# Kernel optimization log

Measured on AMD Instinct MI355X. Metric: run time of the kernel, lower is better.

## Reference

```python
import jax, jax.numpy as jnp
import numpy as np

DIM = 1536
RMS_EPS = 1e-7
LN_EPS = 1e-5


def rmsnorm(x, w):
    ms = jnp.mean(x * x, axis=-1, keepdims=True)
    return x / jnp.sqrt(ms + RMS_EPS) * w


def layernorm(x, w, b):
    mu = jnp.mean(x, axis=-1, keepdims=True)
    var = jnp.mean((x - mu) ** 2, axis=-1, keepdims=True)
    return (x - mu) / jnp.sqrt(var + LN_EPS) * w + b


def linear(x, W, b):
    # W stored as (in, out)
    return jnp.einsum('bnd,df->bnf', x, W) + b


def setup_inputs() -> dict:
    key = jax.random.key(0)
    ks = jax.random.split(key, 32)
    D = DIM
    s = 0.02
    inp = {
        'x': jax.random.normal(ks[0], (2, 4096, D), jnp.float32),
        'text_emb': jax.random.normal(ks[1], (2, 512, D), jnp.float32),
        # norm params
        'sq_w': jnp.ones((D,), jnp.float32),
        'sk_w': jnp.ones((D,), jnp.float32),
        'cq_w': jnp.ones((D,), jnp.float32),
        'ck_w': jnp.ones((D,), jnp.float32),
        'ln_w': jnp.ones((D,), jnp.float32),
        'ln_b': jnp.zeros((D,), jnp.float32),
        # self-attn projections
        'Wq': jax.random.normal(ks[2], (D, D), jnp.float32) * s,
        'bq': jnp.zeros((D,), jnp.float32),
        'Wk': jax.random.normal(ks[3], (D, D), jnp.float32) * s,
        'bk': jnp.zeros((D,), jnp.float32),
        'Wv': jax.random.normal(ks[4], (D, D), jnp.float32) * s,
        'bv': jnp.zeros((D,), jnp.float32),
        'Wo': jax.random.normal(ks[5], (D, D), jnp.float32) * s,
        'bo': jnp.zeros((D,), jnp.float32),
        # cross-attn projections
        'CWq': jax.random.normal(ks[6], (D, D), jnp.float32) * s,
        'Cbq': jnp.zeros((D,), jnp.float32),
        'CWk': jax.random.normal(ks[7], (D, D), jnp.float32) * s,
        'Cbk': jnp.zeros((D,), jnp.float32),
        'CWv': jax.random.normal(ks[8], (D, D), jnp.float32) * s,
        'Cbv': jnp.zeros((D,), jnp.float32),
        'CWo': jax.random.normal(ks[9], (D, D), jnp.float32) * s,
        'Cbo': jnp.zeros((D,), jnp.float32),
        # FFN
        'W1': jax.random.normal(ks[10], (D, 4 * D), jnp.float32) * s,
        'b1': jnp.zeros((4 * D,), jnp.float32),
        'W2': jax.random.normal(ks[11], (4 * D, D), jnp.float32) * s,
        'b2': jnp.zeros((D,), jnp.float32),
    }
    return inp


def reference(x, text_emb, sq_w, sk_w, cq_w, ck_w, ln_w, ln_b,
              Wq, bq, Wk, bk, Wv, bv, Wo, bo,
              CWq, Cbq, CWk, Cbk, CWv, Cbv, CWo, Cbo,
              W1, b1, W2, b2):
    scale = 1.0 / jnp.sqrt(jnp.float32(DIM))  # NOTE: full-dim scale, no head split (faithful)

    # self-attention (single-head over full dim)
    q = linear(rmsnorm(x, sq_w), Wq, bq)
    k = linear(rmsnorm(x, sk_w), Wk, bk)
    v = linear(x, Wv, bv)
    attn = jax.nn.softmax(jnp.einsum('bnd,bmd->bnm', q, k) * scale, axis=-1)
    attn_out = linear(jnp.einsum('bnm,bmd->bnd', attn, v), Wo, bo)

    # cross-attention
    cq = linear(rmsnorm(x, cq_w), CWq, Cbq)
    ck = linear(rmsnorm(text_emb, ck_w), CWk, Cbk)
    cv = linear(text_emb, CWv, Cbv)
    cattn = jax.nn.softmax(jnp.einsum('bnd,bmd->bnm', cq, ck) * scale, axis=-1)
    cross_out = linear(jnp.einsum('bnm,bmd->bnd', cattn, cv), CWo, Cbo)

    # FFN with exact GELU (torch nn.GELU default)
    h = linear(layernorm(x, ln_w, ln_b), W1, b1)
    ffn_out = linear(jax.nn.gelu(h, approximate=False), W2, b2)

    return x + attn_out + cross_out + ffn_out
```

## Files before the change

### kernel.cpp

```cpp
#include <hip/hip_runtime.h>
#include <hip/hip_bf16.h>
#include <cmath>

#define DD 1536
#define FF 6144

typedef __bf16 bf16_t;
typedef __bf16 bf16x8 __attribute__((ext_vector_type(8)));
typedef __bf16 bf16x4 __attribute__((ext_vector_type(4)));
typedef float  f32x4  __attribute__((ext_vector_type(4)));

#define VM0 asm volatile("s_waitcnt vmcnt(0)" ::: "memory")
#define SB  __builtin_amdgcn_sched_barrier(0)
#define LGKM_0 do { asm volatile("s_waitcnt lgkmcnt(0)" :::); SB; } while (0)
#define LGKM_4 do { asm volatile("s_waitcnt lgkmcnt(4)" :::); SB; } while (0)
#define BAR __builtin_amdgcn_s_barrier()

__device__ __forceinline__ void async_load16(const bf16_t* g, bf16_t* l) {
  __builtin_amdgcn_global_load_lds(
      (const __attribute__((address_space(1))) void*)g,
      (__attribute__((address_space(3))) void*)l, 16, 0, 0);
}

__device__ __forceinline__ bf16x8 ds_read128(unsigned int addr) {
  bf16x8 r;
  asm volatile("ds_read_b128 %0, %1" : "=v"(r) : "v"(addr));
  return r;
}

__device__ __forceinline__ void xcd_remap(int& bx, int& by) {
  const int gx = gridDim.x, gy = gridDim.y;
  int wg = by * gx + bx;
  const int nwg = gx * gy;
  const int q = nwg >> 3, r = nwg & 7, xcd = wg & 7, o = wg >> 3;
  wg = (xcd < r ? xcd * (q + 1) : r * (q + 1) + (xcd - r) * q) + o;
  bx = wg % gx;
  by = wg / gx;
}

__global__ __launch_bounds__(256) void transpose_to_bf16(
    const float* __restrict__ W, bf16_t* __restrict__ Wt, int K, int N,
    const float* __restrict__ s, int ldt) {
  __shared__ float tile[32][33];
  const int tx = threadIdx.x, ty = threadIdx.y;
  const int n0 = blockIdx.x * 32, k0 = blockIdx.y * 32;
#pragma unroll
  for (int i = 0; i < 4; i++)
    tile[ty + 8 * i][tx] = W[(size_t)(k0 + ty + 8 * i) * N + n0 + tx];
  __syncthreads();
  const float sc = (s != nullptr) ? s[k0 + tx] : 1.f;
#pragma unroll
  for (int i = 0; i < 4; i++)
    Wt[(size_t)(n0 + ty + 8 * i) * ldt + k0 + tx] = (bf16_t)(tile[tx][ty + 8 * i] * sc);
}

__global__ __launch_bounds__(256) void bias_add2(
    const float* __restrict__ a, const float* __restrict__ b, float* __restrict__ o, int n) {
  const int i = blockIdx.x * 256 + threadIdx.x;
  if (i < n) o[i] = a[i] + b[i];
}

__device__ __forceinline__ void breduce1(float& a) {
#pragma unroll
  for (int off = 32; off; off >>= 1) a += __shfl_xor(a, off);
  __shared__ float sa[4];
  const int w = threadIdx.x >> 6, ln = threadIdx.x & 63;
  if (ln == 0) sa[w] = a;
  __syncthreads();
  a = (sa[0] + sa[1]) + (sa[2] + sa[3]);
  __syncthreads();
}

__device__ __forceinline__ void breduce2(float& a, float& b) {
#pragma unroll
  for (int off = 32; off; off >>= 1) {
    a += __shfl_xor(a, off);
    b += __shfl_xor(b, off);
  }
  __shared__ float sa[4], sb[4];
  const int w = threadIdx.x >> 6, ln = threadIdx.x & 63;
  if (ln == 0) { sa[w] = a; sb[w] = b; }
  __syncthreads();
  a = (sa[0] + sa[1]) + (sa[2] + sa[3]);
  b = (sb[0] + sb[1]) + (sb[2] + sb[3]);
  __syncthreads();
}

__global__ __launch_bounds__(256) void norm_x1(
    const float* __restrict__ x, bf16_t* __restrict__ xr, float* __restrict__ rqinv) {
  const int row = blockIdx.x, t = threadIdx.x;
  const float* p = x + (size_t)row * DD;
  f32x4 v0 = ((const f32x4*)p)[t];
  f32x4 v1 = 0.0f;
  if (t < 128) v1 = ((const f32x4*)p)[256 + t];
  float s2 = 0.f;
#pragma unroll
  for (int e = 0; e < 4; e++) s2 += v0[e] * v0[e];
  if (t < 128) {
#pragma unroll
    for (int e = 0; e < 4; e++) s2 += v1[e] * v1[e];
  }
  breduce1(s2);
  const float ms = s2 * (1.f / DD) + 1e-7f;
  const float rq = rsqrtf(ms);
  if (t == 0) rqinv[row] = sqrtf(ms);
  auto emit = [&](int ci, f32x4 v) {
    bf16x4 orr;
#pragma unroll
    for (int e = 0; e < 4; e++) orr[e] = (bf16_t)(v[e] * rq);
    *(bf16x4*)(xr + (size_t)row * DD + ci * 4) = orr;
  };
  emit(t, v0);
  if (t < 128) emit(256 + t, v1);
}

__global__ __launch_bounds__(256) void norm_ln(
    const float* __restrict__ x, const float* __restrict__ w,
    const float* __restrict__ bb, bf16_t* __restrict__ o) {
  const int row = blockIdx.x, t = threadIdx.x;
  const float* p = x + (size_t)row * DD;
  f32x4 v0 = ((const f32x4*)p)[t];
  f32x4 v1 = 0.0f;
  if (t < 128) v1 = ((const f32x4*)p)[256 + t];
  float s = 0.f, s2 = 0.f;
#pragma unroll
  for (int e = 0; e < 4; e++) { s += v0[e]; s2 += v0[e] * v0[e]; }
  if (t < 128) {
#pragma unroll
    for (int e = 0; e < 4; e++) { s += v1[e]; s2 += v1[e] * v1[e]; }
  }
  breduce2(s, s2);
  const float mu = s * (1.f / DD);
  const float rln = rsqrtf(s2 * (1.f / DD) - mu * mu + 1e-5f);
  auto emit = [&](int ci, f32x4 v) {
    const int i0 = ci * 4;
    bf16x4 ov;
#pragma unroll
    for (int e = 0; e < 4; e++)
      ov[e] = (bf16_t)((v[e] - mu) * rln * w[i0 + e] + bb[i0 + e]);
    *(bf16x4*)(o + (size_t)row * DD + i0) = ov;
  };
  emit(t, v0);
  if (t < 128) emit(256 + t, v1);
}

__global__ __launch_bounds__(256) void norm_t2(
    const float* __restrict__ te, bf16_t* __restrict__ tb, bf16_t* __restrict__ tck) {
  const int row = blockIdx.x, t = threadIdx.x;
  const float* p = te + (size_t)row * DD;
  f32x4 v0 = ((const f32x4*)p)[t];
  f32x4 v1 = 0.0f;
  if (t < 128) v1 = ((const f32x4*)p)[256 + t];
  float s2 = 0.f;
#pragma unroll
  for (int e = 0; e < 4; e++) s2 += v0[e] * v0[e];
  if (t < 128) {
#pragma unroll
    for (int e = 0; e < 4; e++) s2 += v1[e] * v1[e];
  }
  breduce1(s2);
  const float rq = rsqrtf(s2 * (1.f / DD) + 1e-7f);
  auto emit = [&](int ci, f32x4 v) {
    bf16x4 ob, oc;
#pragma unroll
    for (int e = 0; e < 4; e++) {
      ob[e] = (bf16_t)v[e];
      oc[e] = (bf16_t)(v[e] * rq);
    }
    const size_t o = (size_t)row * DD + ci * 4;
    *(bf16x4*)(tb + o) = ob;
    *(bf16x4*)(tck + o) = oc;
  };
  emit(t, v0);
  if (t < 128) emit(256 + t, v1);
}

template <int NC>
__global__ __launch_bounds__(256) void softmax_bf16(bf16_t* __restrict__ S) {
  const int t = threadIdx.x;
  bf16_t* sr = S + (size_t)blockIdx.x * NC;
  constexpr int NV = (NC / 8 + 255) / 256;
  float v[NV][8];
  float mx = -3.4e38f;
#pragma unroll
  for (int i = 0; i < NV; i++) {
    const int idx = t + i * 256;
    if (idx * 8 < NC) {
      bf16x8 b = ((const bf16x8*)sr)[idx];
#pragma unroll
      for (int e = 0; e < 8; e++) {
        v[i][e] = (float)b[e];
        mx = fmaxf(mx, v[i][e]);
      }
    }
  }
#pragma unroll
  for (int off = 32; off; off >>= 1) mx = fmaxf(mx, __shfl_xor(mx, off));
  __shared__ float sm[4];
  const int w = t >> 6, ln = t & 63;
  if (ln == 0) sm[w] = mx;
  __syncthreads();
  mx = fmaxf(fmaxf(sm[0], sm[1]), fmaxf(sm[2], sm[3]));
  __syncthreads();
  float sum = 0.f;
#pragma unroll
  for (int i = 0; i < NV; i++) {
    const int idx = t + i * 256;
    if (idx * 8 < NC) {
#pragma unroll
      for (int e = 0; e < 8; e++) {
        v[i][e] = __expf(v[i][e] - mx);
        sum += v[i][e];
      }
    }
  }
#pragma unroll
  for (int off = 32; off; off >>= 1) sum += __shfl_xor(sum, off);
  __shared__ float ss[4];
  if (ln == 0) ss[w] = sum;
  __syncthreads();
  sum = (ss[0] + ss[1]) + (ss[2] + ss[3]);
  const float inv = 1.f / sum;
#pragma unroll
  for (int i = 0; i < NV; i++) {
    const int idx = t + i * 256;
    if (idx * 8 < NC) {
      bf16x8 o;
#pragma unroll
      for (int e = 0; e < 8; e++) o[e] = (bf16_t)(v[i][e] * inv);
      ((bf16x8*)sr)[idx] = o;
    }
  }
}

enum { EPI_BF16 = 0, EPI_F32_SCALE = 1, EPI_ADD_X = 2, EPI_ACC = 3, EPI_GELU = 4, EPI_TRANS = 5, EPI_BF16S = 6, EPI_PROJ3 = 7 };

template <int EPI>
__device__ __forceinline__ void epi_frag(
    f32x4 v, int r0, int c, const float* bias, void* Cout, const float* Xres,
    int ldc, float scale, int t_ld, int t_bshift, size_t t_bstride) {
  const float bv = (bias != nullptr) ? bias[c] : 0.f;
  if constexpr (EPI == EPI_BF16) {
    bf16_t* C = (bf16_t*)Cout;
#pragma unroll
    for (int r = 0; r < 4; r++) C[(size_t)(r0 + r) * ldc + c] = (bf16_t)(v[r] + bv);
  } else if constexpr (EPI == EPI_F32_SCALE) {
    float* C = (float*)Cout;
#pragma unroll
    for (int r = 0; r < 4; r++) C[(size_t)(r0 + r) * ldc + c] = v[r] * scale;
  } else if constexpr (EPI == EPI_BF16S) {
    bf16_t* C = (bf16_t*)Cout;
#pragma unroll
    for (int r = 0; r < 4; r++) C[(size_t)(r0 + r) * ldc + c] = (bf16_t)(v[r] * scale);
  } else if constexpr (EPI == EPI_ADD_X) {
    float* C = (float*)Cout;
#pragma unroll
    for (int r = 0; r < 4; r++) {
      const size_t ix = (size_t)(r0 + r) * ldc + c;
      C[ix] = Xres[ix] + v[r] + bv;
    }
  } else if constexpr (EPI == EPI_ACC) {
    float* C = (float*)Cout;
#pragma unroll
    for (int r = 0; r < 4; r++) {
      const size_t ix = (size_t)(r0 + r) * ldc + c;
      C[ix] += v[r] + bv;
    }
  } else if constexpr (EPI == EPI_GELU) {
    bf16_t* C = (bf16_t*)Cout;
#pragma unroll
    for (int r = 0; r < 4; r++) {
      const float h = v[r] + bv;
      C[(size_t)(r0 + r) * ldc + c] = (bf16_t)(0.5f * h * (1.f + erff(h * 0.70710678118654752f)));
    }
  } else if constexpr (EPI == EPI_TRANS) {
    const int b = r0 >> t_bshift;
    const int n = r0 & ((1 << t_bshift) - 1);
    bf16_t* C = (bf16_t*)Cout + (size_t)b * t_bstride + (size_t)c * t_ld + n;
    bf16x4 o;
#pragma unroll
    for (int r = 0; r < 4; r++) o[r] = (bf16_t)(v[r] + bv);
    *(bf16x4*)C = o;
  } else {
    bf16_t* base = (bf16_t*)Cout;
    if (c < 1536) {
      const int b = r0 >> 12, n = r0 & 4095;
      bf16_t* C = base + 25165824 + (size_t)b * ((size_t)DD * 4096) + (size_t)c * 4096 + n;
      bf16x4 o;
#pragma unroll
      for (int r = 0; r < 4; r++) o[r] = (bf16_t)(v[r] * Xres[r0 + r] + bv);
      *(bf16x4*)C = o;
    } else if (c < 4608) {
#pragma unroll
      for (int r = 0; r < 4; r++) base[(size_t)(r0 + r) * 3072 + (c - 1536)] = (bf16_t)(v[r] + bv);
    } else {
      bf16_t* C = base + 37748736;
#pragma unroll
      for (int r = 0; r < 4; r++) C[(size_t)(r0 + r) * 1536 + (c - 4608)] = (bf16_t)(v[r] + bv);
    }
  }
}

template <int EPI>
__global__ __launch_bounds__(256) void gemm_bt(
    const bf16_t* __restrict__ A, const bf16_t* __restrict__ B,
    const float* __restrict__ bias, void* __restrict__ Cout,
    const float* __restrict__ Xres,
    int nK, int lda, int ldb, int ldc, float scale,
    int bsh, size_t bstr, int t_ld, int t_bshift, size_t t_bstride) {
  __shared__ __align__(16) bf16_t As[2][128 * 32];
  __shared__ __align__(16) bf16_t Bs[2][128 * 32];
  const int tid = threadIdx.x;
  int bx = blockIdx.x, by = blockIdx.y;
  xcd_remap(bx, by);
  const int m0 = by * 128, n0 = bx * 128;
  const int wave = tid >> 6, lane = tid & 63, l15 = lane & 15, hi = lane >> 4;
  const int wm = wave >> 1, wn = wave & 1;
  const int srow = tid >> 2, scol = (tid & 3) << 3;

  const bf16_t* Bb = bsh ? (B + (size_t)(m0 >> bsh) * bstr) : B;
  const bf16_t* ga = A + (size_t)(m0 + srow) * lda + scol;
  const bf16_t* gb = Bb + (size_t)(n0 + srow) * ldb + scol;
  const int lo = wave * 512;

  f32x4 acc[4][4];
#pragma unroll
  for (int i = 0; i < 4; i++)
#pragma unroll
    for (int j = 0; j < 4; j++) acc[i][j] = 0.0f;

  auto stage = [&](int buf, int kt) {
    const bf16_t* a = ga + (size_t)kt * 32;
    const bf16_t* b = gb + (size_t)kt * 32;
    async_load16(a, &As[buf][lo]);
    async_load16(a + (size_t)64 * lda, &As[buf][2048 + lo]);
    async_load16(b, &Bs[buf][lo]);
    async_load16(b + (size_t)64 * ldb, &Bs[buf][2048 + lo]);
  };

  auto compute = [&](int buf) {
    bf16x8 af[4], bg[4];
#pragma unroll
    for (int i = 0; i < 4; i++)
      af[i] = *(const bf16x8*)&As[buf][(wm * 64 + i * 16 + l15) * 32 + hi * 8];
#pragma unroll
    for (int j = 0; j < 4; j++)
      bg[j] = *(const bf16x8*)&Bs[buf][(wn * 64 + j * 16 + l15) * 32 + hi * 8];
#pragma unroll
    for (int i = 0; i < 4; i++)
#pragma unroll
      for (int j = 0; j < 4; j++)
        acc[i][j] = __builtin_amdgcn_mfma_f32_16x16x32_bf16(af[i], bg[j], acc[i][j], 0, 0, 0);
  };

  stage(0, 0);
  __syncthreads();
  for (int kt = 0; kt < nK; ++kt) {
    if (kt + 1 < nK) stage((kt + 1) & 1, kt + 1);
    compute(kt & 1);
    __syncthreads();
  }

#pragma unroll
  for (int i = 0; i < 4; i++) {
    const int r0 = m0 + wm * 64 + i * 16 + hi * 4;
#pragma unroll
    for (int j = 0; j < 4; j++) {
      const int c = n0 + wn * 64 + j * 16 + l15;
      epi_frag<EPI>(acc[i][j], r0, c, bias, Cout, Xres, ldc, scale, t_ld, t_bshift, t_bstride);
    }
  }
}

template <int EPI>
__global__ __launch_bounds__(512, 2) void gemm8(
    const bf16_t* __restrict__ A, const bf16_t* __restrict__ B,
    const float* __restrict__ bias, void* __restrict__ Cout,
    const float* __restrict__ Xres,
    int nT, int lda, int ldb, int ldc, float scale,
    int bsh, size_t bstr, int t_ld, int t_bshift, size_t t_bstride) {
  __shared__ __align__(16) bf16_t As[2][256 * 64];
  __shared__ __align__(16) bf16_t Bs[2][256 * 64];
  const int tid = threadIdx.x;
  int bx = blockIdx.x, by = blockIdx.y;
  xcd_remap(bx, by);
  const int m0 = by * 256, n0 = bx * 256;
  const int wave = tid >> 6, lane = tid & 63, l15 = lane & 15, hi = lane >> 4;
  const int wm = wave >> 2, wn = wave & 3;

  const int srow = tid >> 3;
  const int scol = ((tid & 7) ^ (srow & 7)) << 3;
  const bf16_t* Bb = bsh ? (B + (size_t)(m0 >> bsh) * bstr) : B;
  const bf16_t* gA = A + (size_t)(m0 + srow) * lda + scol;
  const bf16_t* gB = Bb + (size_t)(n0 + srow) * ldb + scol;
  const int ldst = wave * 512;

  const unsigned swz0 = (unsigned)(((hi ^ (l15 & 7)) << 3) * 2);
  const unsigned swz1 = (unsigned)((((hi + 4) ^ (l15 & 7)) << 3) * 2);
  const unsigned aBase = (unsigned)(size_t)&As[0][0] + (unsigned)((wm * 128 + l15) * 128);
  const unsigned bBase = (unsigned)(size_t)&Bs[0][0] + (unsigned)((wn * 64 + l15) * 128);
  const unsigned a0 = aBase + swz0, a1 = aBase + swz1;
  const unsigned b0 = bBase + swz0, b1 = bBase + swz1;

  f32x4 acc[8][4];
#pragma unroll
  for (int i = 0; i < 8; i++)
#pragma unroll
    for (int j = 0; j < 4; j++) acc[i][j] = 0.0f;

  auto stgA = [&](int t, int half) {
    if (t >= nT) return;
    const int buf = t & 1, r0 = half << 7;
    const size_t kof = (size_t)t * 64;
    async_load16(gA + (size_t)r0 * lda + kof, &As[buf][r0 * 64 + ldst]);
    async_load16(gA + (size_t)(r0 + 64) * lda + kof, &As[buf][(r0 + 64) * 64 + ldst]);
  };
  auto stgB = [&](int t, int half) {
    if (t >= nT) return;
    const int buf = t & 1, r0 = half << 7;
    const size_t kof = (size_t)t * 64;
    async_load16(gB + (size_t)r0 * ldb + kof, &Bs[buf][r0 * 64 + ldst]);
    async_load16(gB + (size_t)(r0 + 64) * ldb + kof, &Bs[buf][(r0 + 64) * 64 + ldst]);
  };

  bf16x8 af[4][2], bg[2][2][2];
  auto LDA = [&](int buf, int mh) {
#pragma unroll
    for (int i = 0; i < 4; i++) {
      const unsigned d = (unsigned)(buf * 32768 + (mh * 4 + i) * 2048);
      af[i][0] = ds_read128(a0 + d);
      af[i][1] = ds_read128(a1 + d);
    }
  };
  auto LDB = [&](int buf, int nh) {
#pragma unroll
    for (int j = 0; j < 2; j++) {
      const unsigned d = (unsigned)(buf * 32768 + (nh * 2 + j) * 2048);
      bg[nh][j][0] = ds_read128(b0 + d);
      bg[nh][j][1] = ds_read128(b1 + d);
    }
  };
  auto MM = [&](int mh, int nh) {
    __builtin_amdgcn_s_setprio(1);
#pragma unroll
    for (int i = 0; i < 4; i++)
#pragma unroll
      for (int j = 0; j < 2; j++)
#pragma unroll
        for (int ks = 0; ks < 2; ks++)
          acc[mh * 4 + i][nh * 2 + j] = __builtin_amdgcn_mfma_f32_16x16x32_bf16(
              af[i][ks], bg[nh][j][ks], acc[mh * 4 + i][nh * 2 + j], 0, 0, 0);
    __builtin_amdgcn_s_setprio(0);
  };

  auto iter = [&](int k, int buf) {
    VM0;
    BAR;
    stgB(k + 1, 0);
    stgB(k + 1, 1);
    stgA(k + 1, 0);
    stgA(k + 1, 1);
    LDA(buf, 0);
    LDB(buf, 0);
    LDB(buf, 1);
    SB;
    LGKM_4;
    MM(0, 0);
    LGKM_0;
    MM(0, 1);
    LDA(buf, 1);
    SB;
    LGKM_0;
    MM(1, 0);
    MM(1, 1);
  };

  stgB(0, 0); stgB(0, 1); stgA(0, 0); stgA(0, 1);

  for (int k = 0; k < nT; k += 2) {
    iter(k, 0);
    iter(k + 1, 1);
  }

#pragma unroll
  for (int fi = 0; fi < 8; fi++) {
    const int r0 = m0 + wm * 128 + fi * 16 + hi * 4;
#pragma unroll
    for (int fj = 0; fj < 4; fj++) {
      const int c = n0 + wn * 64 + fj * 16 + l15;
      epi_frag<EPI>(acc[fi][fj], r0, c, bias, Cout, Xres, ldc, scale, t_ld, t_bshift, t_bstride);
    }
  }
}

extern "C" void kernel_launch(void* const* d_in, const int* in_sizes, int n_in,
                              void* d_out, int out_size, void* d_ws, size_t ws_size,
                              hipStream_t stream) {
  (void)in_sizes; (void)n_in; (void)out_size; (void)ws_size;
  const float* x   = (const float*)d_in[0];
  const float* te  = (const float*)d_in[1];
  const float* sqw = (const float*)d_in[2];
  const float* skw = (const float*)d_in[3];
  const float* cqw = (const float*)d_in[4];
  const float* ckw = (const float*)d_in[5];
  const float* lnw = (const float*)d_in[6];
  const float* lnb = (const float*)d_in[7];
  const float* Wq = (const float*)d_in[8];  const float* bq = (const float*)d_in[9];
  const float* Wk = (const float*)d_in[10]; const float* bk = (const float*)d_in[11];
  const float* Wv = (const float*)d_in[12]; const float* bv = (const float*)d_in[13];
  const float* Wo = (const float*)d_in[14]; const float* bo = (const float*)d_in[15];
  const float* CWq = (const float*)d_in[16]; const float* Cbq = (const float*)d_in[17];
  const float* CWk = (const float*)d_in[18]; const float* Cbk = (const float*)d_in[19];
  const float* CWv = (const float*)d_in[20]; const float* Cbv = (const float*)d_in[21];
  const float* CWo = (const float*)d_in[22]; const float* Cbo = (const float*)d_in[23];
  const float* W1 = (const float*)d_in[24]; const float* b1 = (const float*)d_in[25];
  const float* W2 = (const float*)d_in[26]; const float* b2 = (const float*)d_in[27];
  float* out = (float*)d_out;

  bf16_t* ws = (bf16_t*)d_ws;
  bf16_t* R0 = ws;
  bf16_t* R1 = ws + 9437184;
  bf16_t* R2 = ws + 18874368;
  bf16_t* Tb  = ws + 31457280;
  bf16_t* Tck = ws + 33030144;
  bf16_t* R4 = ws + 34603008;
  bf16_t* R5 = ws + 59768832;
  bf16_t* R6 = ws + 72351744;
  bf16_t* S  = ws;
  float* bcat4 = (float*)(ws + 84934656);
  float* biasm = (float*)(ws + 84946944);
  float* rqinv = (float*)(ws + 84950016);
  bf16_t* CK  = R0;
  bf16_t* CVt = R0 + 1572864;
  bf16_t* Sc  = R0 + 3145728;
  bf16_t* H   = R4;

  const dim3 blk(256), blk8(512), tb(32, 8);
  const float scl = 0.025515518153991442f;

  auto T = [&](const float* W, bf16_t* Wt, int K, int N, const float* s, int ldt) {
    transpose_to_bf16<<<dim3(N / 32, K / 32), tb, 0, stream>>>(W, Wt, K, N, s, ldt);
  };
  auto g8 = [](int M, int N) { return dim3(N / 256, M / 256); };
  auto g4 = [](int M, int N) { return dim3(N / 128, M / 128); };

  hipMemcpyAsync(bcat4,        bv,  DD * sizeof(float), hipMemcpyDeviceToDevice, stream);
  hipMemcpyAsync(bcat4 + DD,   bq,  DD * sizeof(float), hipMemcpyDeviceToDevice, stream);
  hipMemcpyAsync(bcat4 + 2*DD, bk,  DD * sizeof(float), hipMemcpyDeviceToDevice, stream);
  hipMemcpyAsync(bcat4 + 3*DD, Cbq, DD * sizeof(float), hipMemcpyDeviceToDevice, stream);
  bias_add2<<<6, blk, 0, stream>>>(bo, Cbo, biasm, DD);

  norm_x1<<<8192, blk, 0, stream>>>(x, R2, rqinv);

  T(Wv,  R0,               DD, DD, nullptr, DD);
  T(Wq,  R0 + 2359296,     DD, DD, sqw,     DD);
  T(Wk,  R0 + 4718592,     DD, DD, skw,     DD);
  T(CWq, R0 + 7077888,     DD, DD, cqw,     DD);
  gemm8<EPI_PROJ3><<<g8(8192, FF), blk8, 0, stream>>>(R2, R0, bcat4, R4, rqinv,
      24, DD, DD, 3072, 1.f, 0, 0, 0, 0, 0);

  gemm8<EPI_BF16S><<<g8(8192, 4096), blk8, 0, stream>>>(R4 , R4 + DD , nullptr, S, nullptr,
      24, 3072, 3072, 4096, scl, 12, (size_t)4096 * 3072, 0, 0, 0);
  softmax_bf16<4096><<<8192, blk, 0, stream>>>(S);
  gemm8<EPI_BF16><<<g8(8192, DD), blk8, 0, stream>>>(S, R5, nullptr, R4, nullptr,
      64, 4096, 4096, 3072, 1.f, 12, (size_t)DD * 4096, 0, 0, 0);

  norm_t2<<<1024, blk, 0, stream>>>(te, Tb, Tck);
  T(CWk, R1, DD, DD, ckw, DD);
  gemm_bt<EPI_BF16><<<g4(1024, DD), blk, 0, stream>>>(Tck, R1, Cbk, CK, nullptr,
      48, DD, DD, DD, 1.f, 0, 0, 0, 0, 0);
  T(CWv, R1 + 2359296, DD, DD, nullptr, DD);
  gemm_bt<EPI_TRANS><<<g4(1024, DD), blk, 0, stream>>>(Tb, R1 + 2359296, Cbv, CVt, nullptr,
      48, DD, DD, 0, 1.f, 0, 0, 512, 9, (size_t)DD * 512);
  gemm_bt<EPI_BF16S><<<g4(8192, 512), blk, 0, stream>>>(R6 , CK, nullptr, Sc, nullptr,
      48, DD, DD, 512, scl, 12, (size_t)512 * DD, 0, 0, 0);
  softmax_bf16<512><<<8192, blk, 0, stream>>>(Sc);
  gemm8<EPI_BF16><<<g8(8192, DD), blk8, 0, stream>>>(Sc, CVt, nullptr, R4 + 1536, nullptr,
      8, 512, 512, 3072, 1.f, 12, (size_t)DD * 512, 0, 0, 0);

  T(Wo, R1, DD, DD, nullptr, 3072);
  T(CWo, R1 + 1536, DD, DD, nullptr, 3072);
  gemm8<EPI_ADD_X><<<g8(8192, DD), blk8, 0, stream>>>(R4, R1, biasm, out, x,
      48, 3072, 3072, DD, 1.f, 0, 0, 0, 0, 0);

  norm_ln<<<8192, blk, 0, stream>>>(x, lnw, lnb, R2);
  T(W1, R0, DD, FF, nullptr, DD);
  gemm8<EPI_GELU><<<g8(8192, FF), blk8, 0, stream>>>(R2, R0, b1, H, nullptr,
      24, DD, DD, FF, 1.f, 0, 0, 0, 0, 0);
  T(W2, R1, FF, DD, nullptr, FF);
  gemm8<EPI_ACC><<<g8(8192, DD), blk8, 0, stream>>>(H, R1, b2, out, nullptr,
      96, FF, FF, DD, 1.f, 0, 0, 0, 0, 0);
}
```

Before: 1.099 ms.

## Shrink gemm8 to 128x128 tiles with 256 threads and simpler single-phase schedule

The gemm8 kernel moves from 256x256 tiles with 8 waves to 128x128 tiles with 4 waves, halving LDS buffers and accumulators. The interleaved split LDS-read/MFMA schedule with partial lgkmcnt waits is replaced by one full fragment load followed by all MFMAs. This gives more workgroups and possibly higher occupancy, at the cost of lower arithmetic intensity per tile and less overlap of LDS reads with MFMA.

```diff
diff --git a/kernel.cpp b/kernel.cpp
--- a/kernel.cpp
+++ b/kernel.cpp
@@ -13,7 +13,6 @@
 #define VM0 asm volatile("s_waitcnt vmcnt(0)" ::: "memory")
 #define SB  __builtin_amdgcn_sched_barrier(0)
 #define LGKM_0 do { asm volatile("s_waitcnt lgkmcnt(0)" :::); SB; } while (0)
-#define LGKM_4 do { asm volatile("s_waitcnt lgkmcnt(4)" :::); SB; } while (0)
 #define BAR __builtin_amdgcn_s_barrier()
 
 __device__ __forceinline__ void async_load16(const bf16_t* g, bf16_t* l) {
@@ -373,109 +372,91 @@
 }
 
 template <int EPI>
-__global__ __launch_bounds__(512, 2) void gemm8(
+__global__ __launch_bounds__(256, 2) void gemm8(
     const bf16_t* __restrict__ A, const bf16_t* __restrict__ B,
     const float* __restrict__ bias, void* __restrict__ Cout,
     const float* __restrict__ Xres,
     int nT, int lda, int ldb, int ldc, float scale,
     int bsh, size_t bstr, int t_ld, int t_bshift, size_t t_bstride) {
-  __shared__ __align__(16) bf16_t As[2][256 * 64];
-  __shared__ __align__(16) bf16_t Bs[2][256 * 64];
+  __shared__ __align__(16) bf16_t As[2][128 * 64];
+  __shared__ __align__(16) bf16_t Bs[2][128 * 64];
   const int tid = threadIdx.x;
   int bx = blockIdx.x, by = blockIdx.y;
   xcd_remap(bx, by);
-  const int m0 = by * 256, n0 = bx * 256;
+  const int m0 = by * 128, n0 = bx * 128;
   const int wave = tid >> 6, lane = tid & 63, l15 = lane & 15, hi = lane >> 4;
-  const int wm = wave >> 2, wn = wave & 3;
-
-  const int srow = tid >> 3;
-  const int scol = ((tid & 7) ^ (srow & 7)) << 3;
+  const int wm = wave >> 1, wn = wave & 1;
+
+  const int ln8 = lane >> 3, chk = lane & 7;
+  const int scol = (chk ^ ln8) << 3;
   const bf16_t* Bb = bsh ? (B + (size_t)(m0 >> bsh) * bstr) : B;
-  const bf16_t* gA = A + (size_t)(m0 + srow) * lda + scol;
-  const bf16_t* gB = Bb + (size_t)(n0 + srow) * ldb + scol;
-  const int ldst = wave * 512;
-
-  const unsigned swz0 = (unsigned)(((hi ^ (l15 & 7)) << 3) * 2);
-  const unsigned swz1 = (unsigned)((((hi + 4) ^ (l15 & 7)) << 3) * 2);
-  const unsigned aBase = (unsigned)(size_t)&As[0][0] + (unsigned)((wm * 128 + l15) * 128);
+  const bf16_t* gA = A + (size_t)(m0 + wave * 8 + ln8) * lda + scol;
+  const bf16_t* gB = Bb + (size_t)(n0 + wave * 8 + ln8) * ldb + scol;
+  const size_t qrA = (size_t)32 * lda;
+  const size_t qrB = (size_t)32 * ldb;
+
+  const unsigned swz0 = (unsigned)((hi ^ (l15 & 7)) << 4);
+  const unsigned swz1 = (unsigned)(((hi + 4) ^ (l15 & 7)) << 4);
+  const unsigned aBase = (unsigned)(size_t)&As[0][0] + (unsigned)((wm * 64 + l15) * 128);
   const unsigned bBase = (unsigned)(size_t)&Bs[0][0] + (unsigned)((wn * 64 + l15) * 128);
   const unsigned a0 = aBase + swz0, a1 = aBase + swz1;
   const unsigned b0 = bBase + swz0, b1 = bBase + swz1;
 
-  f32x4 acc[8][4];
-#pragma unroll
-  for (int i = 0; i < 8; i++)
+  f32x4 acc[4][4];
+#pragma unroll
+  for (int i = 0; i < 4; i++)
 #pragma unroll
     for (int j = 0; j < 4; j++) acc[i][j] = 0.0f;
 
-  auto stgA = [&](int t, int half) {
+  auto stage = [&](int t) {
     if (t >= nT) return;
-    const int buf = t & 1, r0 = half << 7;
+    const int buf = t & 1;
     const size_t kof = (size_t)t * 64;
-    async_load16(gA + (size_t)r0 * lda + kof, &As[buf][r0 * 64 + ldst]);
-    async_load16(gA + (size_t)(r0 + 64) * lda + kof, &As[buf][(r0 + 64) * 64 + ldst]);
-  };
-  auto stgB = [&](int t, int half) {
-    if (t >= nT) return;
-    const int buf = t & 1, r0 = half << 7;
-    const size_t kof = (size_t)t * 64;
-    async_load16(gB + (size_t)r0 * ldb + kof, &Bs[buf][r0 * 64 + ldst]);
-    async_load16(gB + (size_t)(r0 + 64) * ldb + kof, &Bs[buf][(r0 + 64) * 64 + ldst]);
-  };
-
-  bf16x8 af[4][2], bg[2][2][2];
-  auto LDA = [&](int buf, int mh) {
+#pragma unroll
+    for (int q = 0; q < 4; q++) {
+      async_load16(gA + q * qrA + kof, &As[buf][(q * 4 + wave) * 512]);
+      async_load16(gB + q * qrB + kof, &Bs[buf][(q * 4 + wave) * 512]);
+    }
+  };
+
+  bf16x8 af[4][2], bg[4][2];
+  auto LD = [&](int buf) {
+    const unsigned d = (unsigned)(buf * 16384);
 #pragma unroll
     for (int i = 0; i < 4; i++) {
-      const unsigned d = (unsigned)(buf * 32768 + (mh * 4 + i) * 2048);
-      af[i][0] = ds_read128(a0 + d);
-      af[i][1] = ds_read128(a1 + d);
-    }
-  };
-  auto LDB = [&](int buf, int nh) {
-#pragma unroll
-    for (int j = 0; j < 2; j++) {
-      const unsigned d = (unsigned)(buf * 32768 + (nh * 2 + j) * 2048);
-      bg[nh][j][0] = ds_read128(b0 + d);
-      bg[nh][j][1] = ds_read128(b1 + d);
-    }
-  };
-  auto MM = [&](int mh, int nh) {
+      af[i][0] = ds_read128(a0 + d + i * 2048);
+      af[i][1] = ds_read128(a1 + d + i * 2048);
+    }
+#pragma unroll
+    for (int j = 0; j < 4; j++) {
+      bg[j][0] = ds_read128(b0 + d + j * 2048);
+      bg[j][1] = ds_read128(b1 + d + j * 2048);
+    }
+  };
+  auto MMall = [&]() {
     __builtin_amdgcn_s_setprio(1);
 #pragma unroll
     for (int i = 0; i < 4; i++)
 #pragma unroll
-      for (int j = 0; j < 2; j++)
+      for (int j = 0; j < 4; j++)
 #pragma unroll
         for (int ks = 0; ks < 2; ks++)
-          acc[mh * 4 + i][nh * 2 + j] = __builtin_amdgcn_mfma_f32_16x16x32_bf16(
-              af[i][ks], bg[nh][j][ks], acc[mh * 4 + i][nh * 2 + j], 0, 0, 0);
+          acc[i][j] = __builtin_amdgcn_mfma_f32_16x16x32_bf16(
+              af[i][ks], bg[j][ks], acc[i][j], 0, 0, 0);
     __builtin_amdgcn_s_setprio(0);
   };
 
   auto iter = [&](int k, int buf) {
     VM0;
     BAR;
-    stgB(k + 1, 0);
-    stgB(k + 1, 1);
-    stgA(k + 1, 0);
-    stgA(k + 1, 1);
-    LDA(buf, 0);
-    LDB(buf, 0);
-    LDB(buf, 1);
-    SB;
-    LGKM_4;
-    MM(0, 0);
-    LGKM_0;
-    MM(0, 1);
-    LDA(buf, 1);
+    stage(k + 1);
+    LD(buf);
     SB;
     LGKM_0;
-    MM(1, 0);
-    MM(1, 1);
-  };
-
-  stgB(0, 0); stgB(0, 1); stgA(0, 0); stgA(0, 1);
+    MMall();
+  };
+
+  stage(0);
 
   for (int k = 0; k < nT; k += 2) {
     iter(k, 0);
@@ -483,8 +464,8 @@
   }
 
 #pragma unroll
-  for (int fi = 0; fi < 8; fi++) {
-    const int r0 = m0 + wm * 128 + fi * 16 + hi * 4;
+  for (int fi = 0; fi < 4; fi++) {
+    const int r0 = m0 + wm * 64 + fi * 16 + hi * 4;
 #pragma unroll
     for (int fj = 0; fj < 4; fj++) {
       const int c = n0 + wn * 64 + fj * 16 + l15;
@@ -535,13 +516,13 @@
   bf16_t* Sc  = R0 + 3145728;
   bf16_t* H   = R4;
 
-  const dim3 blk(256), blk8(512), tb(32, 8);
+  const dim3 blk(256), blk8(256), tb(32, 8);
   const float scl = 0.025515518153991442f;
 
   auto T = [&](const float* W, bf16_t* Wt, int K, int N, const float* s, int ldt) {
     transpose_to_bf16<<<dim3(N / 32, K / 32), tb, 0, stream>>>(W, Wt, K, N, s, ldt);
   };
-  auto g8 = [](int M, int N) { return dim3(N / 256, M / 256); };
+  auto g8 = [](int M, int N) { return dim3(N / 128, M / 128); };
   auto g4 = [](int M, int N) { return dim3(N / 128, M / 128); };
 
   hipMemcpyAsync(bcat4,        bv,  DD * sizeof(float), hipMemcpyDeviceToDevice, stream);
```

Result: slower. 1.205 ms (+9.6%).
